# Optimization experiments

Hardware: AMD Instinct MI355X
Metric: run time of the kernel (lower is better)

## Reference

```python
import jax, jax.numpy as jnp
import numpy as np

D_MODEL = 512
N_HEAD = 8
D_K = 64
D_V = 64
D_POS = 4
D_INNER = 2048
TEMPERATURE = D_K ** 0.5
LN_EPS = 1e-6


def _layer_norm(x, g, b):
    mu = jnp.mean(x, axis=-1, keepdims=True)
    var = jnp.var(x, axis=-1, keepdims=True)
    return (x - mu) * jax.lax.rsqrt(var + LN_EPS) * g + b


def setup_inputs() -> dict:
    key = jax.random.key(0)
    ks = jax.random.split(key, 16)
    b, n = 4, 512
    s = lambda fan_in: 1.0 / np.sqrt(fan_in)
    inp = {
        "enc_input": jax.random.normal(ks[0], (b, n, D_MODEL), jnp.float32),
        "pos_mat": jax.random.normal(ks[1], (b, n, n, D_POS), jnp.float32),
        # attention projections (torch Linear convention: [out, in], no bias)
        "w_qs": jax.random.normal(ks[2], (N_HEAD * D_K, D_MODEL), jnp.float32) * s(D_MODEL),
        "w_ks": jax.random.normal(ks[3], (N_HEAD * D_K, D_MODEL), jnp.float32) * s(D_MODEL),
        "w_vs": jax.random.normal(ks[4], (N_HEAD * D_V, D_MODEL), jnp.float32) * s(D_MODEL),
        "w_fc": jax.random.normal(ks[5], (D_MODEL, N_HEAD * D_V), jnp.float32) * s(N_HEAD * D_V),
        # relative-position MLP: pos_dim -> d_k -> d_k
        "rp_w1": jax.random.normal(ks[6], (D_K, D_POS), jnp.float32) * s(D_POS),
        "rp_b1": jnp.zeros((D_K,), jnp.float32),
        "rp_w2": jax.random.normal(ks[7], (D_K, D_K), jnp.float32) * s(D_K),
        "rp_b2": jnp.zeros((D_K,), jnp.float32),
        # layer norms
        "ln1_g": jnp.ones((D_MODEL,), jnp.float32),
        "ln1_b": jnp.zeros((D_MODEL,), jnp.float32),
        "ln2_g": jnp.ones((D_MODEL,), jnp.float32),
        "ln2_b": jnp.zeros((D_MODEL,), jnp.float32),
        # position-wise FFN
        "ffn_w1": jax.random.normal(ks[8], (D_INNER, D_MODEL), jnp.float32) * s(D_MODEL),
        "ffn_b1": jnp.zeros((D_INNER,), jnp.float32),
        "ffn_w2": jax.random.normal(ks[9], (D_MODEL, D_INNER), jnp.float32) * s(D_INNER),
        "ffn_b2": jnp.zeros((D_MODEL,), jnp.float32),
    }
    return inp


def reference(enc_input, pos_mat, w_qs, w_ks, w_vs, w_fc, rp_w1, rp_b1, rp_w2,
              rp_b2, ln1_g, ln1_b, ln2_g, ln2_b, ffn_w1, ffn_b1, ffn_w2, ffn_b2):
    b, n, _ = enc_input.shape
    residual = enc_input
    # project and split heads: [b, n, h, d] -> [b, h, n, d]
    q = (enc_input @ w_qs.T).reshape(b, n, N_HEAD, D_K).transpose(0, 2, 1, 3)
    k = (enc_input @ w_ks.T).reshape(b, n, N_HEAD, D_K).transpose(0, 2, 1, 3)
    v = (enc_input @ w_vs.T).reshape(b, n, N_HEAD, D_V).transpose(0, 2, 1, 3)
    # relative-position embeddings a_k: [b, n, n, d_k]
    a_k = jax.nn.relu if False else None  # placeholder removed
    a_k = (pos_mat @ rp_w1.T + rp_b1) @ rp_w2.T + rp_b2
    # tensor-product attention scores. In torch:
    # attn[b,h,j,i] = sum_d q[b,h,i,d] * k[b,h,j,d] * a_k[b,j,i,d]
    attn = jnp.einsum('bhid,bhjd,bjid->bhji', q, k, a_k) / TEMPERATURE
    attn = jax.nn.softmax(attn, axis=-1)
    out = jnp.matmul(attn, v)  # [b, h, n, d_v]
    out = out.transpose(0, 2, 1, 3).reshape(b, n, N_HEAD * D_V)
    out = out @ w_fc.T + residual
    out = _layer_norm(out, ln1_g, ln1_b)
    # position-wise FFN
    h = jax.nn.relu(out @ ffn_w1.T + ffn_b1)
    out2 = h @ ffn_w2.T + ffn_b2 + out
    out2 = _layer_norm(out2, ln2_g, ln2_b)
    return out2, attn
```

## Files before the change

### kernel.cpp

```cpp
#include <hip/hip_runtime.h>
#include <hip/hip_bf16.h>

typedef unsigned short u16;
typedef unsigned int u32;
typedef __attribute__((ext_vector_type(8))) short short8;
typedef __attribute__((ext_vector_type(4))) short short4v;
typedef __attribute__((ext_vector_type(4))) float floatx4;

__device__ __forceinline__ float bf2f(u16 u) {
    union { u32 u; float f; } x; x.u = ((u32)u) << 16; return x.f;
}
__device__ __forceinline__ u16 f2bf(float f) {
    union { float f; u32 u; } x; x.f = f;
    u32 r = x.u + 0x7FFFu + ((x.u >> 16) & 1u);
    return (u16)(r >> 16);
}

struct Cvt8 {
    const float* src[8];
    u16* dst[8];
    int pre[9];
};

__global__ __launch_bounds__(256) void convert8(Cvt8 a) {
    int total = a.pre[8];
    for (int g = blockIdx.x * 256 + threadIdx.x; g < total; g += gridDim.x * 256) {
        int seg = 0;
        while (a.pre[seg + 1] <= g) seg++;
        int off = g - a.pre[seg];
        float4 f = ((const float4*)a.src[seg])[off];
        short4v o;
        o[0] = (short)f2bf(f.x); o[1] = (short)f2bf(f.y);
        o[2] = (short)f2bf(f.z); o[3] = (short)f2bf(f.w);
        *(short4v*)(a.dst[seg] + (long)off * 4) = o;
    }
}

__global__ void prep_w5(const float* __restrict__ w1, const float* __restrict__ b1,
                        const float* __restrict__ w2, const float* __restrict__ b2,
                        float* __restrict__ W5) {
    int d = threadIdx.x;
    float a0=0.f,a1=0.f,a2=0.f,a3=0.f,ab=0.f;
    for (int e=0;e<64;++e) {
        float w = w2[d*64+e];
        a0 = fmaf(w, w1[e*4+0], a0);
        a1 = fmaf(w, w1[e*4+1], a1);
        a2 = fmaf(w, w1[e*4+2], a2);
        a3 = fmaf(w, w1[e*4+3], a3);
        ab = fmaf(w, b1[e], ab);
    }
    W5[d*8+0]=a0; W5[d*8+1]=a1; W5[d*8+2]=a2; W5[d*8+3]=a3;
    W5[d*8+4]=ab + b2[d];
    W5[d*8+5]=0.f; W5[d*8+6]=0.f; W5[d*8+7]=0.f;
}

enum { MODE_QKV=0, MODE_AV=2, MODE_FC=3, MODE_FFN1=4, MODE_FFN2=5 };

template<int MODE>
__global__ __launch_bounds__(256,2)
void mfma_gemm(const u16* __restrict__ A, const float* __restrict__ Af,
               long sA, int lda,
               const u16* __restrict__ B, int ldb,
               const float* __restrict__ biasf,
               const float* __restrict__ resf,
               const u16* __restrict__ resb,
               void* __restrict__ outp, void* __restrict__ outp2,
               int M, int N, int K)
{
    int bz = blockIdx.z;
    int m0 = blockIdx.x * 64, n0 = blockIdx.y * 64;
    __shared__ __align__(16) u16 As[64*72];
    __shared__ __align__(16) u16 Bs[64*72];
    int tid = threadIdx.x;
    int lane = tid & 63, wave = tid >> 6;
    int wm = (wave >> 1) * 32, wn = (wave & 1) * 32;
    int mrow = lane & 15, quad = lane >> 4;
    floatx4 zz = {0.f,0.f,0.f,0.f};
    floatx4 acc[2][2];
    acc[0][0]=zz; acc[0][1]=zz; acc[1][0]=zz; acc[1][1]=zz;
    int r = tid >> 3;
    int c8 = (tid & 7) * 8;

    long abase = 0, bbase = 0;
    int koff = 0;
    if constexpr (MODE == MODE_AV) {
        abase = (long)bz * sA;
        bbase = (long)bz * (64L * 512L);
    }
    if constexpr (MODE == MODE_FC || MODE == MODE_FFN2) {
        koff = bz * K;
    }

    const u16*   pa  = A  + abase + (long)(m0 + r) * lda + koff + c8;
    const float* paf = Af + abase + (long)(m0 + r) * lda + koff + c8;
    const u16*   pb  = B  + bbase + (long)(n0 + r) * ldb + koff + c8;
    u16* asp = &As[r*72 + c8];
    u16* bsp = &Bs[r*72 + c8];
    const u16* a0p = &As[(wm + mrow)*72];
    const u16* a1p = &As[(wm + 16 + mrow)*72];
    const u16* b0p = &Bs[(wn + mrow)*72];
    const u16* b1p = &Bs[(wn + 16 + mrow)*72];

    short8 ra0, ra1, rb0, rb1;
    floatx4 fa0, fa1, fa2, fa3;
    if constexpr (MODE == MODE_AV) {
        fa0 = *(const floatx4*)(paf);
        fa1 = *(const floatx4*)(paf + 4);
        fa2 = *(const floatx4*)(paf + 32*lda);
        fa3 = *(const floatx4*)(paf + 32*lda + 4);
    } else {
        ra0 = *(const short8*)(pa);
        ra1 = *(const short8*)(pa + 32*lda);
    }
    rb0 = *(const short8*)(pb);
    rb1 = *(const short8*)(pb + 32*ldb);

    for (int k0 = 0; k0 < K; k0 += 64) {
        if constexpr (MODE == MODE_AV) {
            short4v t0,t1,t2,t3;
            #pragma unroll
            for (int e=0;e<4;++e) {
                t0[e]=(short)f2bf(fa0[e]); t1[e]=(short)f2bf(fa1[e]);
                t2[e]=(short)f2bf(fa2[e]); t3[e]=(short)f2bf(fa3[e]);
            }
            *(short4v*)asp           = t0;
            *(short4v*)(asp+4)       = t1;
            *(short4v*)(asp+32*72)   = t2;
            *(short4v*)(asp+32*72+4) = t3;
        } else {
            *(short8*)asp           = ra0;
            *(short8*)(asp + 32*72) = ra1;
        }
        *(short8*)bsp           = rb0;
        *(short8*)(bsp + 32*72) = rb1;
        __syncthreads();
        if (k0 + 64 < K) {
            int kn = k0 + 64;
            if constexpr (MODE == MODE_AV) {
                fa0 = *(const floatx4*)(paf + kn);
                fa1 = *(const floatx4*)(paf + kn + 4);
                fa2 = *(const floatx4*)(paf + kn + 32*lda);
                fa3 = *(const floatx4*)(paf + kn + 32*lda + 4);
            } else {
                ra0 = *(const short8*)(pa + kn);
                ra1 = *(const short8*)(pa + kn + 32*lda);
            }
            rb0 = *(const short8*)(pb + kn);
            rb1 = *(const short8*)(pb + kn + 32*ldb);
        }
        #pragma unroll
        for (int s=0; s<2; ++s) {
            int qo = s*32 + quad*8;
            short8 af0 = *(const short8*)(a0p + qo);
            short8 af1 = *(const short8*)(a1p + qo);
            short8 bf0 = *(const short8*)(b0p + qo);
            short8 bf1 = *(const short8*)(b1p + qo);
            acc[0][0] = __builtin_amdgcn_mfma_f32_16x16x32_bf16(af0, bf0, acc[0][0], 0,0,0);
            acc[0][1] = __builtin_amdgcn_mfma_f32_16x16x32_bf16(af0, bf1, acc[0][1], 0,0,0);
            acc[1][0] = __builtin_amdgcn_mfma_f32_16x16x32_bf16(af1, bf0, acc[1][0], 0,0,0);
            acc[1][1] = __builtin_amdgcn_mfma_f32_16x16x32_bf16(af1, bf1, acc[1][1], 0,0,0);
        }
        __syncthreads();
    }

    if constexpr (MODE == MODE_QKV) {
        if (n0 >= 1024) {
            __shared__ __align__(16) float Cs[64][65];
            #pragma unroll
            for (int im=0; im<2; ++im)
            #pragma unroll
            for (int in=0; in<2; ++in)
            #pragma unroll
            for (int rr=0; rr<4; ++rr)
                Cs[wm + im*16 + quad*4 + rr][wn + in*16 + mrow] = acc[im][in][rr];
            __syncthreads();
            u16* vt = (u16*)outp2;
            int b = m0 >> 9, i0b = m0 & 511, hh = (n0 - 1024) >> 6;
            #pragma unroll
            for (int t=0;t<16;++t) {
                int flat = tid + t*256;
                int d = flat >> 6, il = flat & 63;
                vt[(((long)(b*8 + hh)*64 + d) << 9) + i0b + il] = f2bf(Cs[il][d]);
            }
        } else {
            #pragma unroll
            for (int im=0; im<2; ++im)
            #pragma unroll
            for (int in=0; in<2; ++in)
            #pragma unroll
            for (int rr=0; rr<4; ++rr) {
                int mm = m0 + wm + im*16 + quad*4 + rr;
                int nn = n0 + wn + in*16 + mrow;
                int b = mm >> 9, i = mm & 511;
                int sel = nn >> 9, hh = (nn >> 6) & 7, d = nn & 63;
                ((u16*)outp)[(long)sel*1048576 +
                             (((long)(b*8 + hh)*512 + i) << 6) + d]
                    = f2bf(acc[im][in][rr]);
            }
        }
    } else {
        #pragma unroll
        for (int im=0; im<2; ++im)
        #pragma unroll
        for (int in=0; in<2; ++in)
        #pragma unroll
        for (int rr=0; rr<4; ++rr) {
            int mm = m0 + wm + im*16 + quad*4 + rr;
            int nn = n0 + wn + in*16 + mrow;
            float v = acc[im][in][rr];
            if constexpr (MODE == MODE_AV) {
                int b = bz >> 3, hh = bz & 7;
                ((u16*)outp)[((long)(b*512 + mm)) * 512 + hh*64 + nn] = f2bf(v);
            } else if constexpr (MODE == MODE_FC) {
                float* OP = (float*)(bz ? outp2 : outp);
                OP[(long)mm*512 + nn] = bz ? v : v + resf[(long)mm*512 + nn];
            } else if constexpr (MODE == MODE_FFN1) {
                float t = v + biasf[nn];
                ((u16*)outp)[(long)mm*2048 + nn] = f2bf(t > 0.f ? t : 0.f);
            } else {
                float* OP = (float*)(bz ? outp2 : outp);
                OP[(long)mm*512 + nn] =
                    bz ? v : v + biasf[nn] + bf2f(resb[(long)mm*512 + nn]);
            }
        }
    }
}

__global__ __launch_bounds__(256,2)
void attn_scores(const u16* __restrict__ qws, const u16* __restrict__ kws,
                 const u16* __restrict__ pos, const float* __restrict__ W5g,
                 float* __restrict__ attn_of)
{
    int jt = blockIdx.x, h = blockIdx.y, b = blockIdx.z;
    int j0 = jt * 16;
    int bh = b*8 + h;
    const u16* qb = qws + (long)bh * 512 * 64;
    const u16* kb = kws + (long)bh * 512 * 64;
    __shared__ __align__(16) float W5s[512];
    __shared__ __align__(16) float S[16*516];
    __shared__ __align__(16) float redm[16][17];
    __shared__ __align__(16) float reds[16][17];
    __shared__ float rinvs[16];
    int tid = threadIdx.x;
    int lane = tid & 63, wave = tid >> 6;
    int m = lane & 15, quad = lane >> 4;
    if (tid < 64) {
        #pragma unroll
        for (int p=0;p<8;++p) W5s[tid*8+p] = W5g[tid*8+p];
    }
    __syncthreads();
    short8 af[5][2];
    #pragma unroll
    for (int s=0; s<2; ++s) {
        short8 kf = *(const short8*)(kb + (long)(j0 + m)*64 + s*32 + quad*8);
        float kv[8];
        #pragma unroll
        for (int e=0;e<8;++e) kv[e] = bf2f((u16)kf[e]);
        int db = s*32 + quad*8;
        #pragma unroll
        for (int p=0;p<5;++p) {
            short8 t;
            #pragma unroll
            for (int e=0;e<8;++e) t[e] = (short)f2bf(kv[e] * W5s[(db+e)*8 + p]);
            af[p][s] = t;
        }
    }
    floatx4 zz = {0.f,0.f,0.f,0.f};
    for (int it = wave*8; it < wave*8 + 8; ++it) {
        int i0 = it * 16;
        short8 bf0 = *(const short8*)(qb + (long)(i0 + m)*64 + quad*8);
        short8 bf1 = *(const short8*)(qb + (long)(i0 + m)*64 + 32 + quad*8);
        floatx4 a0 = __builtin_amdgcn_mfma_f32_16x16x32_bf16(af[0][0], bf0, zz, 0,0,0);
        floatx4 a1 = __builtin_amdgcn_mfma_f32_16x16x32_bf16(af[1][0], bf0, zz, 0,0,0);
        floatx4 a2 = __builtin_amdgcn_mfma_f32_16x16x32_bf16(af[2][0], bf0, zz, 0,0,0);
        floatx4 a3 = __builtin_amdgcn_mfma_f32_16x16x32_bf16(af[3][0], bf0, zz, 0,0,0);
        floatx4 a4 = __builtin_amdgcn_mfma_f32_16x16x32_bf16(af[4][0], bf0, zz, 0,0,0);
        a0 = __builtin_amdgcn_mfma_f32_16x16x32_bf16(af[0][1], bf1, a0, 0,0,0);
        a1 = __builtin_amdgcn_mfma_f32_16x16x32_bf16(af[1][1], bf1, a1, 0,0,0);
        a2 = __builtin_amdgcn_mfma_f32_16x16x32_bf16(af[2][1], bf1, a2, 0,0,0);
        a3 = __builtin_amdgcn_mfma_f32_16x16x32_bf16(af[3][1], bf1, a3, 0,0,0);
        a4 = __builtin_amdgcn_mfma_f32_16x16x32_bf16(af[4][1], bf1, a4, 0,0,0);
        long pb0 = (((long)(b*512 + j0 + quad*4))*512 + i0 + m) * 4;
        #pragma unroll
        for (int rr=0; rr<4; ++rr) {
            uint2 pp = *(const uint2*)&pos[pb0 + (long)rr*2048];
            float p0 = bf2f((u16)(pp.x & 0xffff));
            float p1 = bf2f((u16)(pp.x >> 16));
            float p2 = bf2f((u16)(pp.y & 0xffff));
            float p3 = bf2f((u16)(pp.y >> 16));
            float sv = a4[rr];
            sv = fmaf(p0, a0[rr], sv);
            sv = fmaf(p1, a1[rr], sv);
            sv = fmaf(p2, a2[rr], sv);
            sv = fmaf(p3, a3[rr], sv);
            S[(quad*4 + rr)*516 + i0 + m] = sv * 0.125f;
        }
    }
    __syncthreads();
    int j = tid >> 4, sub = tid & 15;
    float mx = -1e30f;
    for (int t=0;t<32;++t) mx = fmaxf(mx, S[j*516 + sub + t*16]);
    redm[j][sub] = mx;
    __syncthreads();
    float mval = redm[j][0];
    #pragma unroll
    for (int p=1;p<16;++p) mval = fmaxf(mval, redm[j][p]);
    float sum = 0.f;
    for (int t=0;t<32;++t) {
        int i = sub + t*16;
        float e = __expf(S[j*516 + i] - mval);
        S[j*516 + i] = e;
        sum += e;
    }
    reds[j][sub] = sum;
    __syncthreads();
    float tot = 0.f;
    #pragma unroll
    for (int p=0;p<16;++p) tot += reds[j][p];
    if (sub == 0) rinvs[j] = 1.0f / tot;
    __syncthreads();
    long rowbase = ((long)bh * 512 + j0) * 512;
    for (int t=0;t<16;++t) {
        int idx = (tid + t*256) * 2;
        int jj = idx >> 9, i = idx & 511;
        float ri = rinvs[jj];
        float2 f2; f2.x = S[jj*516 + i]*ri; f2.y = S[jj*516 + i + 1]*ri;
        *(float2*)&attn_of[rowbase + (long)jj*512 + i] = f2;
    }
}

__global__ __launch_bounds__(256)
void ln_kernel(const float* __restrict__ x, const float* __restrict__ x2,
               const float* __restrict__ g, const float* __restrict__ bb,
               u16* __restrict__ outb, float* __restrict__ outf)
{
    int row = blockIdx.x, tid = threadIdx.x;
    const float* xr = x + (long)row * 512;
    float v0 = xr[tid*2], v1 = xr[tid*2+1];
    if (x2) {
        const float* x2r = x2 + (long)row * 512;
        v0 += x2r[tid*2];
        v1 += x2r[tid*2+1];
    }
    __shared__ float r1[256], r2[256];
    r1[tid] = v0 + v1;
    r2[tid] = v0*v0 + v1*v1;
    __syncthreads();
    for (int sft=128; sft>0; sft>>=1) {
        if (tid < sft) { r1[tid] += r1[tid+sft]; r2[tid] += r2[tid+sft]; }
        __syncthreads();
    }
    float mu = r1[0] * (1.0f/512.0f);
    float var = r2[0] * (1.0f/512.0f) - mu*mu;
    float rs = rsqrtf(var + 1e-6f);
    float y0 = fmaf((v0-mu)*rs, g[tid*2],   bb[tid*2]);
    float y1 = fmaf((v1-mu)*rs, g[tid*2+1], bb[tid*2+1]);
    if (outf) {
        float2 f2; f2.x = y0; f2.y = y1;
        *(float2*)&outf[(long)row*512 + tid*2] = f2;
    }
    if (outb) {
        ((u32*)outb)[row*256 + tid] = (u32)f2bf(y0) | ((u32)f2bf(y1) << 16);
    }
}

extern "C" void kernel_launch(void* const* d_in, const int* in_sizes, int n_in,
                              void* d_out, int out_size, void* d_ws, size_t ws_size,
                              hipStream_t stream)
{
    const float* enc_f  = (const float*)d_in[0];
    const float* rp_w1  = (const float*)d_in[6];
    const float* rp_b1  = (const float*)d_in[7];
    const float* rp_w2  = (const float*)d_in[8];
    const float* rp_b2  = (const float*)d_in[9];
    const float* ln1_g  = (const float*)d_in[10];
    const float* ln1_b  = (const float*)d_in[11];
    const float* ln2_g  = (const float*)d_in[12];
    const float* ln2_b  = (const float*)d_in[13];
    const float* ffn_b1 = (const float*)d_in[15];
    const float* ffn_b2 = (const float*)d_in[17];

    char* ws = (char*)d_ws;
    const size_t MB = 1048576ul;
    u16* enc_c = (u16*)(ws + 0);
    u16* pos_c = (u16*)(ws + 2*MB);
    u16* wq_c  = (u16*)(ws + 10*MB);
    u16* wk_c  = (u16*)(ws + 10*MB + 524288);
    u16* wv_c  = (u16*)(ws + 11*MB);
    u16* wfc_c = (u16*)(ws + 11*MB + 524288);
    u16* fw1_c = (u16*)(ws + 12*MB);
    u16* fw2_c = (u16*)(ws + 14*MB);
    u16* qws   = (u16*)(ws + 16*MB);
    u16* vtws  = (u16*)(ws + 20*MB);
    u16* hws   = (u16*)(ws + 2*MB);
    u16* aows  = (u16*)(ws + 16*MB);
    u16* ln1ws = (u16*)(ws + 18*MB);
    float* p1fc = (float*)(ws + 2*MB);
    float* p1f2 = (float*)(ws + 10*MB);
    float* W5   = (float*)(ws + 22*MB);

    float* out0_f = (float*)d_out;
    float* attn_f = out0_f + 1048576;
    float* res    = out0_f;

    dim3 blk(256);

    Cvt8 ca;
    const float* srcs[8] = { enc_f, (const float*)d_in[1], (const float*)d_in[2],
                             (const float*)d_in[3], (const float*)d_in[4],
                             (const float*)d_in[5], (const float*)d_in[14],
                             (const float*)d_in[16] };
    u16* dsts[8] = { enc_c, pos_c, wq_c, wk_c, wv_c, wfc_c, fw1_c, fw2_c };
    int sizes4[8] = { 262144, 1048576, 65536, 65536, 65536, 65536, 262144, 262144 };
    int pre = 0;
    for (int i = 0; i < 8; ++i) {
        ca.src[i] = srcs[i]; ca.dst[i] = dsts[i]; ca.pre[i] = pre;
        pre += sizes4[i];
    }
    ca.pre[8] = pre;
    convert8<<<dim3(8192), blk, 0, stream>>>(ca);

    prep_w5<<<dim3(1), dim3(64), 0, stream>>>(rp_w1, rp_b1, rp_w2, rp_b2, W5);

    mfma_gemm<MODE_QKV><<<dim3(32,24,1), blk, 0, stream>>>(
        enc_c, nullptr, 0L, 512, wq_c, 512, nullptr, nullptr, nullptr,
        (void*)qws, (void*)vtws, 2048, 1536, 512);

    attn_scores<<<dim3(32,8,4), blk, 0, stream>>>(qws, qws + 1048576, pos_c, W5, attn_f);

    mfma_gemm<MODE_AV><<<dim3(8,1,32), blk, 0, stream>>>(
        nullptr, attn_f, 512L*512L, 512, vtws, 512, nullptr, nullptr, nullptr,
        (void*)aows, nullptr, 512, 64, 512);

    mfma_gemm<MODE_FC><<<dim3(32,8,2), blk, 0, stream>>>(
        aows, nullptr, 0L, 512, wfc_c, 512, nullptr, enc_f, nullptr,
        (void*)res, (void*)p1fc, 2048, 512, 256);
    ln_kernel<<<dim3(2048), blk, 0, stream>>>(res, p1fc, ln1_g, ln1_b, ln1ws, nullptr);

    mfma_gemm<MODE_FFN1><<<dim3(32,32,1), blk, 0, stream>>>(
        ln1ws, nullptr, 0L, 512, fw1_c, 512, ffn_b1, nullptr, nullptr,
        (void*)hws, nullptr, 2048, 2048, 512);

    mfma_gemm<MODE_FFN2><<<dim3(32,8,2), blk, 0, stream>>>(
        hws, nullptr, 0L, 2048, fw2_c, 2048, ffn_b2, nullptr, ln1ws,
        (void*)res, (void*)p1f2, 2048, 512, 1024);
    ln_kernel<<<dim3(2048), blk, 0, stream>>>(res, p1f2, ln2_g, ln2_b, nullptr, out0_f);
}
```

Baseline: 205.3 us.

## Fuse attention-times-V into score kernel and use 128-row tiles for QKV/FFN1

The separate AV GEMM is removed. The attention-score kernel now multiplies its normalized softmax tile (still held in shared memory) by V^T with MFMA and writes the head outputs directly. This avoids re-reading the fp32 attention matrix from global memory and saves one launch. QKV and FFN1 GEMMs move to a 128x64 tile kernel for more reuse per block, at the cost of more registers and shared memory and fewer blocks.

```diff
diff --git a/kernel.cpp b/kernel.cpp
--- a/kernel.cpp
+++ b/kernel.cpp
@@ -54,18 +54,128 @@
     W5[d*8+5]=0.f; W5[d*8+6]=0.f; W5[d*8+7]=0.f;
 }
 
-enum { MODE_QKV=0, MODE_AV=2, MODE_FC=3, MODE_FFN1=4, MODE_FFN2=5 };
+enum { MODE_QKV=0, MODE_FFN1=1, MODE_FC=2, MODE_FFN2=3 };
 
 template<int MODE>
 __global__ __launch_bounds__(256,2)
-void mfma_gemm(const u16* __restrict__ A, const float* __restrict__ Af,
-               long sA, int lda,
-               const u16* __restrict__ B, int ldb,
-               const float* __restrict__ biasf,
-               const float* __restrict__ resf,
-               const u16* __restrict__ resb,
-               void* __restrict__ outp, void* __restrict__ outp2,
-               int M, int N, int K)
+void gemm128(const u16* __restrict__ A, int lda,
+             const u16* __restrict__ B, int ldb,
+             const float* __restrict__ biasf,
+             void* __restrict__ outp, void* __restrict__ outp2,
+             int K)
+{
+    int m0 = blockIdx.x * 128, n0 = blockIdx.y * 64;
+    __shared__ __align__(16) u16 As[128*72];
+    __shared__ __align__(16) u16 Bs[64*72];
+    int tid = threadIdx.x;
+    int lane = tid & 63, wave = tid >> 6;
+    int wm = (wave >> 1) * 64, wn = (wave & 1) * 32;
+    int mrow = lane & 15, quad = lane >> 4;
+    floatx4 zz = {0.f,0.f,0.f,0.f};
+    floatx4 acc[4][2];
+    #pragma unroll
+    for (int i=0;i<4;++i) { acc[i][0]=zz; acc[i][1]=zz; }
+
+    int rA = tid >> 1, cA = (tid & 1) * 32;
+    int rB = tid >> 2, cB = (tid & 3) * 16;
+    const u16* pa = A + (long)(m0 + rA) * lda + cA;
+    const u16* pb = B + (long)(n0 + rB) * ldb + cB;
+    u16* asp = &As[rA*72 + cA];
+    u16* bsp = &Bs[rB*72 + cB];
+
+    short8 ra[4], rb[2];
+    #pragma unroll
+    for (int i=0;i<4;++i) ra[i] = *(const short8*)(pa + 8*i);
+    #pragma unroll
+    for (int i=0;i<2;++i) rb[i] = *(const short8*)(pb + 8*i);
+
+    for (int k0 = 0; k0 < K; k0 += 64) {
+        #pragma unroll
+        for (int i=0;i<4;++i) *(short8*)(asp + 8*i) = ra[i];
+        #pragma unroll
+        for (int i=0;i<2;++i) *(short8*)(bsp + 8*i) = rb[i];
+        __syncthreads();
+        if (k0 + 64 < K) {
+            int kn = k0 + 64;
+            #pragma unroll
+            for (int i=0;i<4;++i) ra[i] = *(const short8*)(pa + kn + 8*i);
+            #pragma unroll
+            for (int i=0;i<2;++i) rb[i] = *(const short8*)(pb + kn + 8*i);
+        }
+        #pragma unroll
+        for (int s=0; s<2; ++s) {
+            int qo = s*32 + quad*8;
+            short8 bf0 = *(const short8*)(&Bs[(wn + mrow)*72 + qo]);
+            short8 bf1 = *(const short8*)(&Bs[(wn + 16 + mrow)*72 + qo]);
+            #pragma unroll
+            for (int mt=0; mt<4; ++mt) {
+                short8 af = *(const short8*)(&As[(wm + mt*16 + mrow)*72 + qo]);
+                acc[mt][0] = __builtin_amdgcn_mfma_f32_16x16x32_bf16(af, bf0, acc[mt][0], 0,0,0);
+                acc[mt][1] = __builtin_amdgcn_mfma_f32_16x16x32_bf16(af, bf1, acc[mt][1], 0,0,0);
+            }
+        }
+        __syncthreads();
+    }
+
+    if constexpr (MODE == MODE_QKV) {
+        if (n0 >= 1024) {
+            __shared__ __align__(16) float Cs[128][65];
+            #pragma unroll
+            for (int mt=0; mt<4; ++mt)
+            #pragma unroll
+            for (int nt=0; nt<2; ++nt)
+            #pragma unroll
+            for (int rr=0; rr<4; ++rr)
+                Cs[wm + mt*16 + quad*4 + rr][wn + nt*16 + mrow] = acc[mt][nt][rr];
+            __syncthreads();
+            u16* vt = (u16*)outp2;
+            int b = m0 >> 9, i0b = m0 & 511, hh = (n0 - 1024) >> 6;
+            #pragma unroll
+            for (int t=0;t<32;++t) {
+                int flat = tid + t*256;
+                int d = flat >> 7, il = flat & 127;
+                vt[(((long)(b*8 + hh)*64 + d) << 9) + i0b + il] = f2bf(Cs[il][d]);
+            }
+        } else {
+            #pragma unroll
+            for (int mt=0; mt<4; ++mt)
+            #pragma unroll
+            for (int nt=0; nt<2; ++nt)
+            #pragma unroll
+            for (int rr=0; rr<4; ++rr) {
+                int mm = m0 + wm + mt*16 + quad*4 + rr;
+                int nn = n0 + wn + nt*16 + mrow;
+                int b = mm >> 9, i = mm & 511;
+                int sel = nn >> 9, hh = (nn >> 6) & 7, d = nn & 63;
+                ((u16*)outp)[(long)sel*1048576 +
+                             (((long)(b*8 + hh)*512 + i) << 6) + d]
+                    = f2bf(acc[mt][nt][rr]);
+            }
+        }
+    } else {
+        #pragma unroll
+        for (int mt=0; mt<4; ++mt)
+        #pragma unroll
+        for (int nt=0; nt<2; ++nt)
+        #pragma unroll
+        for (int rr=0; rr<4; ++rr) {
+            int mm = m0 + wm + mt*16 + quad*4 + rr;
+            int nn = n0 + wn + nt*16 + mrow;
+            float t = acc[mt][nt][rr] + biasf[nn];
+            ((u16*)outp)[(long)mm*2048 + nn] = f2bf(t > 0.f ? t : 0.f);
+        }
+    }
+}
+
+template<int MODE>
+__global__ __launch_bounds__(256,2)
+void gemm64(const u16* __restrict__ A, int lda,
+            const u16* __restrict__ B, int ldb,
+            const float* __restrict__ biasf,
+            const float* __restrict__ resf,
+            const u16* __restrict__ resb,
+            void* __restrict__ outp, void* __restrict__ outp2,
+            int K)
 {
     int bz = blockIdx.z;
     int m0 = blockIdx.x * 64, n0 = blockIdx.y * 64;
@@ -78,73 +188,30 @@
     floatx4 zz = {0.f,0.f,0.f,0.f};
     floatx4 acc[2][2];
     acc[0][0]=zz; acc[0][1]=zz; acc[1][0]=zz; acc[1][1]=zz;
-    int r = tid >> 3;
-    int c8 = (tid & 7) * 8;
-
-    long abase = 0, bbase = 0;
-    int koff = 0;
-    if constexpr (MODE == MODE_AV) {
-        abase = (long)bz * sA;
-        bbase = (long)bz * (64L * 512L);
-    }
-    if constexpr (MODE == MODE_FC || MODE == MODE_FFN2) {
-        koff = bz * K;
-    }
-
-    const u16*   pa  = A  + abase + (long)(m0 + r) * lda + koff + c8;
-    const float* paf = Af + abase + (long)(m0 + r) * lda + koff + c8;
-    const u16*   pb  = B  + bbase + (long)(n0 + r) * ldb + koff + c8;
+    int r = tid >> 3, c8 = (tid & 7) * 8;
+    int koff = bz * K;
+    const u16* pa = A + (long)(m0 + r) * lda + koff + c8;
+    const u16* pb = B + (long)(n0 + r) * ldb + koff + c8;
     u16* asp = &As[r*72 + c8];
     u16* bsp = &Bs[r*72 + c8];
     const u16* a0p = &As[(wm + mrow)*72];
     const u16* a1p = &As[(wm + 16 + mrow)*72];
     const u16* b0p = &Bs[(wn + mrow)*72];
     const u16* b1p = &Bs[(wn + 16 + mrow)*72];
-
-    short8 ra0, ra1, rb0, rb1;
-    floatx4 fa0, fa1, fa2, fa3;
-    if constexpr (MODE == MODE_AV) {
-        fa0 = *(const floatx4*)(paf);
-        fa1 = *(const floatx4*)(paf + 4);
-        fa2 = *(const floatx4*)(paf + 32*lda);
-        fa3 = *(const floatx4*)(paf + 32*lda + 4);
-    } else {
-        ra0 = *(const short8*)(pa);
-        ra1 = *(const short8*)(pa + 32*lda);
-    }
-    rb0 = *(const short8*)(pb);
-    rb1 = *(const short8*)(pb + 32*ldb);
-
+    short8 ra0 = *(const short8*)(pa);
+    short8 ra1 = *(const short8*)(pa + 32*lda);
+    short8 rb0 = *(const short8*)(pb);
+    short8 rb1 = *(const short8*)(pb + 32*ldb);
     for (int k0 = 0; k0 < K; k0 += 64) {
-        if constexpr (MODE == MODE_AV) {
-            short4v t0,t1,t2,t3;
-            #pragma unroll
-            for (int e=0;e<4;++e) {
-                t0[e]=(short)f2bf(fa0[e]); t1[e]=(short)f2bf(fa1[e]);
-                t2[e]=(short)f2bf(fa2[e]); t3[e]=(short)f2bf(fa3[e]);
-            }
-            *(short4v*)asp           = t0;
-            *(short4v*)(asp+4)       = t1;
-            *(short4v*)(asp+32*72)   = t2;
-            *(short4v*)(asp+32*72+4) = t3;
-        } else {
-            *(short8*)asp           = ra0;
-            *(short8*)(asp + 32*72) = ra1;
-        }
+        *(short8*)asp           = ra0;
+        *(short8*)(asp + 32*72) = ra1;
         *(short8*)bsp           = rb0;
         *(short8*)(bsp + 32*72) = rb1;
         __syncthreads();
         if (k0 + 64 < K) {
             int kn = k0 + 64;
-            if constexpr (MODE == MODE_AV) {
-                fa0 = *(const floatx4*)(paf + kn);
-                fa1 = *(const floatx4*)(paf + kn + 4);
-                fa2 = *(const floatx4*)(paf + kn + 32*lda);
-                fa3 = *(const floatx4*)(paf + kn + 32*lda + 4);
-            } else {
-                ra0 = *(const short8*)(pa + kn);
-                ra1 = *(const short8*)(pa + kn + 32*lda);
-            }
+            ra0 = *(const short8*)(pa + kn);
+            ra1 = *(const short8*)(pa + kn + 32*lda);
             rb0 = *(const short8*)(pb + kn);
             rb1 = *(const short8*)(pb + kn + 32*ldb);
         }
@@ -162,66 +229,21 @@
         }
         __syncthreads();
     }
-
-    if constexpr (MODE == MODE_QKV) {
-        if (n0 >= 1024) {
-            __shared__ __align__(16) float Cs[64][65];
-            #pragma unroll
-            for (int im=0; im<2; ++im)
-            #pragma unroll
-            for (int in=0; in<2; ++in)
-            #pragma unroll
-            for (int rr=0; rr<4; ++rr)
-                Cs[wm + im*16 + quad*4 + rr][wn + in*16 + mrow] = acc[im][in][rr];
-            __syncthreads();
-            u16* vt = (u16*)outp2;
-            int b = m0 >> 9, i0b = m0 & 511, hh = (n0 - 1024) >> 6;
-            #pragma unroll
-            for (int t=0;t<16;++t) {
-                int flat = tid + t*256;
-                int d = flat >> 6, il = flat & 63;
-                vt[(((long)(b*8 + hh)*64 + d) << 9) + i0b + il] = f2bf(Cs[il][d]);
-            }
+    #pragma unroll
+    for (int im=0; im<2; ++im)
+    #pragma unroll
+    for (int in=0; in<2; ++in)
+    #pragma unroll
+    for (int rr=0; rr<4; ++rr) {
+        int mm = m0 + wm + im*16 + quad*4 + rr;
+        int nn = n0 + wn + in*16 + mrow;
+        float v = acc[im][in][rr];
+        float* OP = (float*)(bz ? outp2 : outp);
+        if constexpr (MODE == MODE_FC) {
+            OP[(long)mm*512 + nn] = bz ? v : v + resf[(long)mm*512 + nn];
         } else {
-            #pragma unroll
-            for (int im=0; im<2; ++im)
-            #pragma unroll
-            for (int in=0; in<2; ++in)
-            #pragma unroll
-            for (int rr=0; rr<4; ++rr) {
-                int mm = m0 + wm + im*16 + quad*4 + rr;
-                int nn = n0 + wn + in*16 + mrow;
-                int b = mm >> 9, i = mm & 511;
-                int sel = nn >> 9, hh = (nn >> 6) & 7, d = nn & 63;
-                ((u16*)outp)[(long)sel*1048576 +
-                             (((long)(b*8 + hh)*512 + i) << 6) + d]
-                    = f2bf(acc[im][in][rr]);
-            }
-        }
-    } else {
-        #pragma unroll
-        for (int im=0; im<2; ++im)
-        #pragma unroll
-        for (int in=0; in<2; ++in)
-        #pragma unroll
-        for (int rr=0; rr<4; ++rr) {
-            int mm = m0 + wm + im*16 + quad*4 + rr;
-            int nn = n0 + wn + in*16 + mrow;
-            float v = acc[im][in][rr];
-            if constexpr (MODE == MODE_AV) {
-                int b = bz >> 3, hh = bz & 7;
-                ((u16*)outp)[((long)(b*512 + mm)) * 512 + hh*64 + nn] = f2bf(v);
-            } else if constexpr (MODE == MODE_FC) {
-                float* OP = (float*)(bz ? outp2 : outp);
-                OP[(long)mm*512 + nn] = bz ? v : v + resf[(long)mm*512 + nn];
-            } else if constexpr (MODE == MODE_FFN1) {
-                float t = v + biasf[nn];
-                ((u16*)outp)[(long)mm*2048 + nn] = f2bf(t > 0.f ? t : 0.f);
-            } else {
-                float* OP = (float*)(bz ? outp2 : outp);
-                OP[(long)mm*512 + nn] =
-                    bz ? v : v + biasf[nn] + bf2f(resb[(long)mm*512 + nn]);
-            }
+            OP[(long)mm*512 + nn] =
+                bz ? v : v + biasf[nn] + bf2f(resb[(long)mm*512 + nn]);
         }
     }
 }
@@ -229,6 +251,7 @@
 __global__ __launch_bounds__(256,2)
 void attn_scores(const u16* __restrict__ qws, const u16* __restrict__ kws,
                  const u16* __restrict__ pos, const float* __restrict__ W5g,
+                 const u16* __restrict__ vtws, u16* __restrict__ aows,
                  float* __restrict__ attn_of)
 {
     int jt = blockIdx.x, h = blockIdx.y, b = blockIdx.z;
@@ -327,6 +350,23 @@
         float2 f2; f2.x = S[jj*516 + i]*ri; f2.y = S[jj*516 + i + 1]*ri;
         *(float2*)&attn_of[rowbase + (long)jj*512 + i] = f2;
     }
+    float rim = rinvs[m];
+    const u16* vb = vtws + (long)bh * 64 * 512 + (long)(wave*16 + m)*512;
+    floatx4 oacc = zz;
+    for (int kk = 0; kk < 16; ++kk) {
+        short8 afr;
+        #pragma unroll
+        for (int e=0;e<8;++e)
+            afr[e] = (short)f2bf(S[m*516 + kk*32 + quad*8 + e] * rim);
+        short8 bfr = *(const short8*)(vb + kk*32 + quad*8);
+        oacc = __builtin_amdgcn_mfma_f32_16x16x32_bf16(afr, bfr, oacc, 0,0,0);
+    }
+    int dd = wave*16 + m;
+    #pragma unroll
+    for (int rr=0; rr<4; ++rr) {
+        int jj = quad*4 + rr;
+        aows[((long)(b*512 + j0 + jj))*512 + h*64 + dd] = f2bf(oacc[rr]);
+    }
 }
 
 __global__ __launch_bounds__(256)
@@ -391,9 +431,10 @@
     u16* fw1_c = (u16*)(ws + 12*MB);
     u16* fw2_c = (u16*)(ws + 14*MB);
     u16* qws   = (u16*)(ws + 16*MB);
+    u16* kws   = (u16*)(ws + 18*MB);
     u16* vtws  = (u16*)(ws + 20*MB);
+    u16* aows  = (u16*)(ws + 0);
     u16* hws   = (u16*)(ws + 2*MB);
-    u16* aows  = (u16*)(ws + 16*MB);
     u16* ln1ws = (u16*)(ws + 18*MB);
     float* p1fc = (float*)(ws + 2*MB);
     float* p1f2 = (float*)(ws + 10*MB);
@@ -422,27 +463,22 @@
 
     prep_w5<<<dim3(1), dim3(64), 0, stream>>>(rp_w1, rp_b1, rp_w2, rp_b2, W5);
 
-    mfma_gemm<MODE_QKV><<<dim3(32,24,1), blk, 0, stream>>>(
-        enc_c, nullptr, 0L, 512, wq_c, 512, nullptr, nullptr, nullptr,
-        (void*)qws, (void*)vtws, 2048, 1536, 512);
-
-    attn_scores<<<dim3(32,8,4), blk, 0, stream>>>(qws, qws + 1048576, pos_c, W5, attn_f);
-
-    mfma_gemm<MODE_AV><<<dim3(8,1,32), blk, 0, stream>>>(
-        nullptr, attn_f, 512L*512L, 512, vtws, 512, nullptr, nullptr, nullptr,
-        (void*)aows, nullptr, 512, 64, 512);
-
-    mfma_gemm<MODE_FC><<<dim3(32,8,2), blk, 0, stream>>>(
-        aows, nullptr, 0L, 512, wfc_c, 512, nullptr, enc_f, nullptr,
-        (void*)res, (void*)p1fc, 2048, 512, 256);
+    gemm128<MODE_QKV><<<dim3(16,24,1), blk, 0, stream>>>(
+        enc_c, 512, wq_c, 512, nullptr, (void*)qws, (void*)vtws, 512);
+
+    attn_scores<<<dim3(32,8,4), blk, 0, stream>>>(
+        qws, kws, pos_c, W5, vtws, aows, attn_f);
+
+    gemm64<MODE_FC><<<dim3(32,8,2), blk, 0, stream>>>(
+        aows, 512, wfc_c, 512, nullptr, enc_f, nullptr,
+        (void*)res, (void*)p1fc, 256);
     ln_kernel<<<dim3(2048), blk, 0, stream>>>(res, p1fc, ln1_g, ln1_b, ln1ws, nullptr);
 
-    mfma_gemm<MODE_FFN1><<<dim3(32,32,1), blk, 0, stream>>>(
-        ln1ws, nullptr, 0L, 512, fw1_c, 512, ffn_b1, nullptr, nullptr,
-        (void*)hws, nullptr, 2048, 2048, 512);
-
-    mfma_gemm<MODE_FFN2><<<dim3(32,8,2), blk, 0, stream>>>(
-        hws, nullptr, 0L, 2048, fw2_c, 2048, ffn_b2, nullptr, ln1ws,
-        (void*)res, (void*)p1f2, 2048, 512, 1024);
+    gemm128<MODE_FFN1><<<dim3(16,32,1), blk, 0, stream>>>(
+        ln1ws, 512, fw1_c, 512, ffn_b1, (void*)hws, nullptr, 512);
+
+    gemm64<MODE_FFN2><<<dim3(32,8,2), blk, 0, stream>>>(
+        hws, 2048, fw2_c, 2048, ffn_b2, nullptr, ln1ws,
+        (void*)res, (void*)p1f2, 1024);
     ln_kernel<<<dim3(2048), blk, 0, stream>>>(res, p1f2, ln2_g, ln2_b, nullptr, out0_f);
 }
```

Result: faster. 198.5 us (-3.3%).
